# Performance work log

Measured on AMD Instinct MI355X. Metric: run time of the kernel, lower is better.

Reference implementation:

```python
import jax, jax.numpy as jnp
import numpy as np

HEADS = 16
WINDOW = 256
OVERLAP = WINDOW // 8  # 32, matches window_size // 8


def setup_inputs() -> dict:
    key = jax.random.key(0)
    ks = jax.random.split(key, 8)
    n, L, E = 4, 4096, 1024
    d = E // HEADS
    return {
        "values": jax.random.normal(ks[0], (n, L, E), jnp.float32),
        "keys": jax.random.normal(ks[1], (n, L, E), jnp.float32),
        "queries": jax.random.normal(ks[2], (n, L, E), jnp.float32),
        "mask": jnp.ones((n, L), jnp.int32),
        "Wv": jax.random.normal(ks[3], (d, d), jnp.float32) * 0.125,
        "Wk": jax.random.normal(ks[4], (d, d), jnp.float32) * 0.125,
        "Wq": jax.random.normal(ks[5], (d, d), jnp.float32) * 0.125,
        "Wf": jax.random.normal(ks[6], (E, E), jnp.float32) * 0.03125,
        "bf": jnp.zeros((E,), jnp.float32),
    }


def reference(values, keys, queries, mask, Wv, Wk, Wq, Wf, bf):
    n, L, E = queries.shape
    d = E // HEADS
    nW = L // WINDOW            # number of (non-overlapping) query windows
    K = WINDOW + 2 * OVERLAP    # halo-extended key window length

    # per-head linear projections (torch Linear: x @ W^T)
    v = jnp.einsum('nlhd,ed->nlhe', values.reshape(n, L, HEADS, d), Wv)
    k = jnp.einsum('nlhd,ed->nlhe', keys.reshape(n, L, HEADS, d), Wk)
    q = jnp.einsum('nlhd,ed->nlhe', queries.reshape(n, L, HEADS, d), Wq)

    # pad keys/values by the halo; invalid (padded) positions masked with -inf
    kp = jnp.pad(k, ((0, 0), (OVERLAP, OVERLAP), (0, 0), (0, 0)))
    vp = jnp.pad(v, ((0, 0), (OVERLAP, OVERLAP), (0, 0), (0, 0)))
    idx = jnp.arange(nW)[:, None] * WINDOW + jnp.arange(K)[None, :]  # [nW, K] padded coords
    kw = kp[:, idx]  # [n, nW, K, h, d]
    vw = vp[:, idx]
    qw = q.reshape(n, nW, WINDOW, HEADS, d)

    en = jnp.einsum('nwqhd,nwkhd->nwhqk', qw, kw)  # [n, nW, h, WINDOW, K]
    # query-row mask fill (original: masked_fill with -1e10 before scaling)
    qmask = mask.reshape(n, nW, WINDOW)
    en = jnp.where(qmask[:, :, None, :, None] == 0, jnp.float32(-1e10), en)
    # halo positions outside the true sequence get exactly zero weight (= slicing)
    key_valid = (idx >= OVERLAP) & (idx < OVERLAP + L)  # [nW, K]
    en = jnp.where(key_valid[None, :, None, None, :], en, -jnp.inf)

    att = jax.nn.softmax(en / (d ** 0.5), axis=-1)
    out = jnp.einsum('nwhqk,nwkhd->nwqhd', att, vw).reshape(n, L, E)
    return out @ Wf.T + bf
```

## Files before the change

### kernel.cpp

```cpp
#include <hip/hip_runtime.h>
#include <hip/hip_bf16.h>
#include <stdint.h>

typedef unsigned int uint;
typedef unsigned short ushort;

#define NB 4
#define SL 4096
#define EMB 1024
#define NH 16
#define DH 64
#define WIN 256
#define OVL 32
#define NW 16
#define NTOK (NB * SL)

typedef __attribute__((ext_vector_type(8))) short short8;
typedef __attribute__((ext_vector_type(4))) float float4v;

#define AS1 __attribute__((address_space(1)))
#define AS3 __attribute__((address_space(3)))

__device__ __forceinline__ float bf2f(ushort s) { return __uint_as_float((uint)s << 16); }
__device__ __forceinline__ ushort f2bf(float x) {
  uint u = __float_as_uint(x);
  u += 0x7fffu + ((u >> 16) & 1u);
  return (ushort)(u >> 16);
}
__device__ __forceinline__ uint packbf(float a, float b) {
  return (uint)f2bf(a) | ((uint)f2bf(b) << 16);
}

__global__ __launch_bounds__(256) void qkv_proj_mfma(
    const float* __restrict__ qin, const float* __restrict__ kin,
    const float* __restrict__ vin,
    const float* __restrict__ Wq, const float* __restrict__ Wk,
    const float* __restrict__ Wv,
    ushort* __restrict__ qo, ushort* __restrict__ ko, ushort* __restrict__ vo) {
  __shared__ alignas(16) ushort sx[256 * 72];
  __shared__ alignas(16) ushort sw[64 * 72];
  const int t = threadIdx.x;
  const int wid = t >> 6, lane = t & 63, quad = lane >> 4, l16 = lane & 15;
  const int p = blockIdx.z, h = blockIdx.y;
  const int tok0 = blockIdx.x * 256;

  const float* src = (p == 0) ? qin : ((p == 1) ? kin : vin);
  const float* W   = (p == 0) ? Wq  : ((p == 1) ? Wk  : Wv);
  ushort* dst      = (p == 0) ? qo  : ((p == 1) ? ko  : vo);

  for (int i = t; i < 1024; i += 256) {
    int e = i >> 4, c4 = i & 15;
    float4 f = *(const float4*)(W + e * 64 + c4 * 4);
    uint2 u;
    u.x = packbf(f.x, f.y);
    u.y = packbf(f.z, f.w);
    *(uint2*)&sw[e * 72 + c4 * 4] = u;
  }
  for (int i = t; i < 4096; i += 256) {
    int tok = i >> 4, c4 = i & 15;
    float4 f = *(const float4*)(src + (size_t)(tok0 + tok) * EMB + h * DH + c4 * 4);
    uint2 u;
    u.x = packbf(f.x, f.y);
    u.y = packbf(f.z, f.w);
    *(uint2*)&sx[tok * 72 + c4 * 4] = u;
  }
  __syncthreads();

  short8 wa[4][2], xb[4][2];
#pragma unroll
  for (int mt = 0; mt < 4; ++mt)
#pragma unroll
    for (int kh = 0; kh < 2; ++kh)
      wa[mt][kh] = *(const short8*)&sw[(mt * 16 + l16) * 72 + kh * 32 + quad * 8];
#pragma unroll
  for (int nt = 0; nt < 4; ++nt)
#pragma unroll
    for (int kh = 0; kh < 2; ++kh)
      xb[nt][kh] = *(const short8*)&sx[(wid * 64 + nt * 16 + l16) * 72 + kh * 32 + quad * 8];

  float4v acc[4][4];
#pragma unroll
  for (int i = 0; i < 4; ++i)
#pragma unroll
    for (int j = 0; j < 4; ++j) acc[i][j] = (float4v){0.f, 0.f, 0.f, 0.f};
#pragma unroll
  for (int kh = 0; kh < 2; ++kh)
#pragma unroll
    for (int mt = 0; mt < 4; ++mt)
#pragma unroll
      for (int nt = 0; nt < 4; ++nt)
        acc[mt][nt] = __builtin_amdgcn_mfma_f32_16x16x32_bf16(
            wa[mt][kh], xb[nt][kh], acc[mt][nt], 0, 0, 0);

  __syncthreads();
#pragma unroll
  for (int mt = 0; mt < 4; ++mt)
#pragma unroll
    for (int nt = 0; nt < 4; ++nt) {
      uint2 u;
      u.x = packbf(acc[mt][nt][0], acc[mt][nt][1]);
      u.y = packbf(acc[mt][nt][2], acc[mt][nt][3]);
      *(uint2*)&sx[(wid * 64 + nt * 16 + l16) * 72 + mt * 16 + quad * 4] = u;
    }
  __syncthreads();

  {
    const int tokg = tok0 + t;
    const int nb = tokg >> 12, l = tokg & 4095;
    uint4* orow = (uint4*)(dst + ((size_t)(nb * NH + h) * SL + l) * DH);
#pragma unroll
    for (int j = 0; j < 8; ++j) orow[j] = *(const uint4*)&sx[t * 72 + j * 8];
  }
}

__global__ __launch_bounds__(256, 3) void attn_win_mfma(
    const ushort* __restrict__ qws, const ushort* __restrict__ kws,
    const ushort* __restrict__ vws, const int* __restrict__ mask,
    ushort* __restrict__ att) {
  __shared__ alignas(16) ushort sk[64 * 72];
  __shared__ alignas(16) ushort svT[64 * 72];
  __shared__ alignas(16) ushort sp[4][64 * 40];

  const int t = threadIdx.x;
  const int wid = t >> 6, lane = t & 63, quad = lane >> 4, l16 = lane & 15;
  const int bid = blockIdx.x;
  const int h = bid & 15, w = (bid >> 4) & 15, nb = bid >> 8;
  const size_t headbase = (size_t)(nb * NH + h) * SL;
  const int q0 = w * WIN + wid * 64;

  const float CSC = 0.18033688f;
  float sc[4];
#pragma unroll
  for (int qt = 0; qt < 4; ++qt)
    sc[qt] = mask[nb * SL + q0 + qt * 16 + l16] ? CSC : 0.f;

  short8 qf[4][2];
#pragma unroll
  for (int qt = 0; qt < 4; ++qt)
#pragma unroll
    for (int kd = 0; kd < 2; ++kd)
      qf[qt][kd] = *(const short8*)(qws + (headbase + q0 + qt * 16 + l16) * DH +
                                    kd * 32 + quad * 8);

  float4v Of[4][4];
#pragma unroll
  for (int dt = 0; dt < 4; ++dt)
#pragma unroll
    for (int qt = 0; qt < 4; ++qt) Of[dt][qt] = (float4v){0.f, 0.f, 0.f, 0.f};
  float lsum[4] = {0.f, 0.f, 0.f, 0.f};

  ushort* spw = &sp[wid][0];
  const int gk0 = w * WIN - OVL;

  for (int c = 0; c < 5; ++c) {
    __syncthreads();
    const int cbase = gk0 + c * 64;
    for (int s = t; s < 512; s += 256) {
      int key = s & 63, dj = s >> 6;
      int gk = cbase + key;
      uint4 kq = make_uint4(0u, 0u, 0u, 0u);
      uint4 vq = make_uint4(0u, 0u, 0u, 0u);
      if ((unsigned)gk < (unsigned)SL) {
        kq = *(const uint4*)(kws + (headbase + gk) * DH + dj * 8);
        vq = *(const uint4*)(vws + (headbase + gk) * DH + dj * 8);
      }
      *(uint4*)&sk[key * 72 + dj * 8] = kq;
      svT[(dj * 8 + 0) * 72 + key] = (ushort)(vq.x & 0xffffu);
      svT[(dj * 8 + 1) * 72 + key] = (ushort)(vq.x >> 16);
      svT[(dj * 8 + 2) * 72 + key] = (ushort)(vq.y & 0xffffu);
      svT[(dj * 8 + 3) * 72 + key] = (ushort)(vq.y >> 16);
      svT[(dj * 8 + 4) * 72 + key] = (ushort)(vq.z & 0xffffu);
      svT[(dj * 8 + 5) * 72 + key] = (ushort)(vq.z >> 16);
      svT[(dj * 8 + 6) * 72 + key] = (ushort)(vq.w & 0xffffu);
      svT[(dj * 8 + 7) * 72 + key] = (ushort)(vq.w >> 16);
    }
    __syncthreads();

    const bool kmask = (cbase < 0) || (cbase + 64 > SL);

#pragma unroll
    for (int khk = 0; khk < 2; ++khk) {
      float4v Sf[2][4];
#pragma unroll
      for (int kt = 0; kt < 2; ++kt)
#pragma unroll
        for (int qt = 0; qt < 4; ++qt) Sf[kt][qt] = (float4v){0.f, 0.f, 0.f, 0.f};
#pragma unroll
      for (int kd = 0; kd < 2; ++kd) {
        short8 kf[2];
#pragma unroll
        for (int kt = 0; kt < 2; ++kt)
          kf[kt] = *(const short8*)&sk[(khk * 32 + kt * 16 + l16) * 72 +
                                       kd * 32 + quad * 8];
#pragma unroll
        for (int kt = 0; kt < 2; ++kt)
#pragma unroll
          for (int qt = 0; qt < 4; ++qt)
            Sf[kt][qt] = __builtin_amdgcn_mfma_f32_16x16x32_bf16(
                kf[kt], qf[qt][kd], Sf[kt][qt], 0, 0, 0);
      }

#pragma unroll
      for (int kt = 0; kt < 2; ++kt)
#pragma unroll
        for (int qt = 0; qt < 4; ++qt) {
          float p[4];
#pragma unroll
          for (int r = 0; r < 4; ++r)
            p[r] = exp2f(Sf[kt][qt][r] * sc[qt]);
          if (kmask) {
#pragma unroll
            for (int r = 0; r < 4; ++r) {
              const int gkey = cbase + khk * 32 + kt * 16 + quad * 4 + r;
              if ((unsigned)gkey >= (unsigned)SL) p[r] = 0.f;
            }
          }
          uint2 u;
          u.x = packbf(p[0], p[1]);
          u.y = packbf(p[2], p[3]);
          lsum[qt] += (bf2f((ushort)(u.x & 0xffffu)) + bf2f((ushort)(u.x >> 16))) +
                      (bf2f((ushort)(u.y & 0xffffu)) + bf2f((ushort)(u.y >> 16)));
          *(uint2*)&spw[(qt * 16 + l16) * 40 + kt * 16 + quad * 4] = u;
        }

      short8 vf[4], pf[4];
#pragma unroll
      for (int dt = 0; dt < 4; ++dt)
        vf[dt] = *(const short8*)&svT[(dt * 16 + l16) * 72 + khk * 32 + quad * 8];
#pragma unroll
      for (int qt = 0; qt < 4; ++qt)
        pf[qt] = *(const short8*)&spw[(qt * 16 + l16) * 40 + quad * 8];
#pragma unroll
      for (int dt = 0; dt < 4; ++dt)
#pragma unroll
        for (int qt = 0; qt < 4; ++qt)
          Of[dt][qt] = __builtin_amdgcn_mfma_f32_16x16x32_bf16(
              vf[dt], pf[qt], Of[dt][qt], 0, 0, 0);
    }
  }

#pragma unroll
  for (int qt = 0; qt < 4; ++qt) {
    lsum[qt] += __shfl_xor(lsum[qt], 16);
    lsum[qt] += __shfl_xor(lsum[qt], 32);
  }

#pragma unroll
  for (int qt = 0; qt < 4; ++qt) {
    const float inv = 1.f / lsum[qt];
    const size_t token = (size_t)nb * SL + q0 + qt * 16 + l16;
#pragma unroll
    for (int dt = 0; dt < 4; ++dt) {
      uint2 u;
      u.x = packbf(Of[dt][qt][0] * inv, Of[dt][qt][1] * inv);
      u.y = packbf(Of[dt][qt][2] * inv, Of[dt][qt][3] * inv);
      *(uint2*)(att + token * EMB + h * DH + dt * 16 + quad * 4) = u;
    }
  }
}

__global__ __launch_bounds__(256) void wf_cvt(const float* __restrict__ Wf,
                                              ushort* __restrict__ o) {
  const int i = blockIdx.x * 256 + threadIdx.x;
  float4 f = ((const float4*)Wf)[i];
  uint2 u;
  u.x = packbf(f.x, f.y);
  u.y = packbf(f.z, f.w);
  ((uint2*)o)[i] = u;
}

#define GBK 64
__global__ __launch_bounds__(256) void final_gemm_mfma(
    const ushort* __restrict__ A, const ushort* __restrict__ Bt,
    const float* __restrict__ bias, float* __restrict__ C) {
  __shared__ alignas(16) ushort sA[128 * GBK];
  __shared__ alignas(16) ushort sB[128 * GBK];
  const int t = threadIdx.x;
  const int wid = t >> 6, lane = t & 63, quad = lane >> 4, l16 = lane & 15;
  const int n0 = blockIdx.x * 128, m0 = blockIdx.y * 128;
  const int wm = (wid & 1) * 64, wn = (wid >> 1) * 64;

  float4v acc[4][4];
#pragma unroll
  for (int i = 0; i < 4; ++i)
#pragma unroll
    for (int j = 0; j < 4; ++j) acc[i][j] = (float4v){0.f, 0.f, 0.f, 0.f};

  const int arow = lane >> 3;
  const int acol = (lane & 7) * 8;

  for (int k0 = 0; k0 < EMB; k0 += GBK) {
    __syncthreads();
#pragma unroll
    for (int seg = 0; seg < 4; ++seg) {
      const int r = wid * 32 + seg * 8;
      __builtin_amdgcn_global_load_lds(
          (AS1 const void*)(A + (size_t)(m0 + r + arow) * EMB + k0 + acol),
          (AS3 void*)&sA[r * GBK], 16, 0, 0);
      __builtin_amdgcn_global_load_lds(
          (AS1 const void*)(Bt + (size_t)(n0 + r + arow) * EMB + k0 + acol),
          (AS3 void*)&sB[r * GBK], 16, 0, 0);
    }
    __syncthreads();
#pragma unroll
    for (int kk = 0; kk < GBK; kk += 32) {
      short8 af[4], bfr[4];
#pragma unroll
      for (int i = 0; i < 4; ++i)
        af[i] = *(const short8*)&sA[(wm + i * 16 + l16) * GBK + kk + quad * 8];
#pragma unroll
      for (int j = 0; j < 4; ++j)
        bfr[j] = *(const short8*)&sB[(wn + j * 16 + l16) * GBK + kk + quad * 8];
#pragma unroll
      for (int i = 0; i < 4; ++i)
#pragma unroll
        for (int j = 0; j < 4; ++j)
          acc[i][j] = __builtin_amdgcn_mfma_f32_16x16x32_bf16(af[i], bfr[j],
                                                              acc[i][j], 0, 0, 0);
    }
  }

  float bv[4];
#pragma unroll
  for (int j = 0; j < 4; ++j) bv[j] = bias[n0 + wn + j * 16 + l16];
#pragma unroll
  for (int i = 0; i < 4; ++i)
#pragma unroll
    for (int j = 0; j < 4; ++j)
#pragma unroll
      for (int r = 0; r < 4; ++r)
        C[(size_t)(m0 + wm + i * 16 + quad * 4 + r) * EMB + n0 + wn + j * 16 +
          l16] = acc[i][j][r] + bv[j];
}

extern "C" void kernel_launch(void* const* d_in, const int* in_sizes, int n_in,
                              void* d_out, int out_size, void* d_ws,
                              size_t ws_size, hipStream_t stream) {
  const float* values  = (const float*)d_in[0];
  const float* keys    = (const float*)d_in[1];
  const float* queries = (const float*)d_in[2];
  const int*   mask    = (const int*)d_in[3];
  const float* Wv = (const float*)d_in[4];
  const float* Wk = (const float*)d_in[5];
  const float* Wq = (const float*)d_in[6];
  const float* Wf = (const float*)d_in[7];
  const float* bfv = (const float*)d_in[8];
  float* out = (float*)d_out;

  ushort* ws = (ushort*)d_ws;
  ushort* q_ws = ws;
  ushort* k_ws = ws + (size_t)16777216;
  ushort* v_ws = ws + (size_t)33554432;
  ushort* a_ws = ws + (size_t)50331648;
  ushort* wf_bf = q_ws;

  qkv_proj_mfma<<<dim3(NTOK / 256, NH, 3), 256, 0, stream>>>(
      queries, keys, values, Wq, Wk, Wv, q_ws, k_ws, v_ws);
  attn_win_mfma<<<NB * NW * NH, 256, 0, stream>>>(q_ws, k_ws, v_ws, mask, a_ws);
  wf_cvt<<<1024, 256, 0, stream>>>(Wf, wf_bf);
  final_gemm_mfma<<<dim3(EMB / 128, NTOK / 128), 256, 0, stream>>>(a_ws, wf_bf,
                                                                   bfv, out);
}
```

Baseline: 465.9 us.

## Store V pre-transposed from projection and stage attention output through LDS

The projection kernel now writes V in a head-major transposed [d, L] layout by computing the transposed product and staging it through LDS. This lets the attention kernel load V^T tiles with vector loads instead of scalar scattered LDS writes. The attention output is also staged in shared memory so each thread writes a full 128-byte row, and the projection grid order is swapped so heads vary fastest. The cost is extra syncs and LDS traffic in the epilogues, and V halo loads now work at 8-key granularity.

```diff
diff --git a/kernel.cpp b/kernel.cpp
--- a/kernel.cpp
+++ b/kernel.cpp
@@ -37,12 +37,16 @@
     const float* __restrict__ Wq, const float* __restrict__ Wk,
     const float* __restrict__ Wv,
     ushort* __restrict__ qo, ushort* __restrict__ ko, ushort* __restrict__ vo) {
-  __shared__ alignas(16) ushort sx[256 * 72];
-  __shared__ alignas(16) ushort sw[64 * 72];
+  __shared__ alignas(16) ushort smem[256 * 72 + 64 * 72];
+  ushort* sx = smem;
+  ushort* sw = smem + 256 * 72;
+  ushort* sxT = smem;
+
   const int t = threadIdx.x;
   const int wid = t >> 6, lane = t & 63, quad = lane >> 4, l16 = lane & 15;
-  const int p = blockIdx.z, h = blockIdx.y;
-  const int tok0 = blockIdx.x * 256;
+  const int p = blockIdx.z, h = blockIdx.x;
+  const int tok0 = blockIdx.y * 256;
+  const int nb = tok0 >> 12, l0 = tok0 & 4095;
 
   const float* src = (p == 0) ? qin : ((p == 1) ? kin : vin);
   const float* W   = (p == 0) ? Wq  : ((p == 1) ? Wk  : Wv);
@@ -66,50 +70,72 @@
   }
   __syncthreads();
 
-  short8 wa[4][2], xb[4][2];
-#pragma unroll
-  for (int mt = 0; mt < 4; ++mt)
+  short8 wfr[4][2], xfr[4][2];
+#pragma unroll
+  for (int et = 0; et < 4; ++et)
 #pragma unroll
     for (int kh = 0; kh < 2; ++kh)
-      wa[mt][kh] = *(const short8*)&sw[(mt * 16 + l16) * 72 + kh * 32 + quad * 8];
-#pragma unroll
-  for (int nt = 0; nt < 4; ++nt)
+      wfr[et][kh] = *(const short8*)&sw[(et * 16 + l16) * 72 + kh * 32 + quad * 8];
+#pragma unroll
+  for (int tt = 0; tt < 4; ++tt)
 #pragma unroll
     for (int kh = 0; kh < 2; ++kh)
-      xb[nt][kh] = *(const short8*)&sx[(wid * 64 + nt * 16 + l16) * 72 + kh * 32 + quad * 8];
+      xfr[tt][kh] = *(const short8*)&sx[(wid * 64 + tt * 16 + l16) * 72 + kh * 32 + quad * 8];
 
   float4v acc[4][4];
 #pragma unroll
   for (int i = 0; i < 4; ++i)
 #pragma unroll
     for (int j = 0; j < 4; ++j) acc[i][j] = (float4v){0.f, 0.f, 0.f, 0.f};
-#pragma unroll
-  for (int kh = 0; kh < 2; ++kh)
-#pragma unroll
-    for (int mt = 0; mt < 4; ++mt)
-#pragma unroll
-      for (int nt = 0; nt < 4; ++nt)
-        acc[mt][nt] = __builtin_amdgcn_mfma_f32_16x16x32_bf16(
-            wa[mt][kh], xb[nt][kh], acc[mt][nt], 0, 0, 0);
-
-  __syncthreads();
-#pragma unroll
-  for (int mt = 0; mt < 4; ++mt)
-#pragma unroll
-    for (int nt = 0; nt < 4; ++nt) {
-      uint2 u;
-      u.x = packbf(acc[mt][nt][0], acc[mt][nt][1]);
-      u.y = packbf(acc[mt][nt][2], acc[mt][nt][3]);
-      *(uint2*)&sx[(wid * 64 + nt * 16 + l16) * 72 + mt * 16 + quad * 4] = u;
-    }
-  __syncthreads();
-
-  {
-    const int tokg = tok0 + t;
-    const int nb = tokg >> 12, l = tokg & 4095;
-    uint4* orow = (uint4*)(dst + ((size_t)(nb * NH + h) * SL + l) * DH);
+
+  if (p != 2) {
+#pragma unroll
+    for (int kh = 0; kh < 2; ++kh)
+#pragma unroll
+      for (int et = 0; et < 4; ++et)
+#pragma unroll
+        for (int tt = 0; tt < 4; ++tt)
+          acc[et][tt] = __builtin_amdgcn_mfma_f32_16x16x32_bf16(
+              wfr[et][kh], xfr[tt][kh], acc[et][tt], 0, 0, 0);
+    __syncthreads();
+#pragma unroll
+    for (int et = 0; et < 4; ++et)
+#pragma unroll
+      for (int tt = 0; tt < 4; ++tt) {
+        uint2 u;
+        u.x = packbf(acc[et][tt][0], acc[et][tt][1]);
+        u.y = packbf(acc[et][tt][2], acc[et][tt][3]);
+        *(uint2*)&sx[(wid * 64 + tt * 16 + l16) * 72 + et * 16 + quad * 4] = u;
+      }
+    __syncthreads();
+    uint4* orow = (uint4*)(dst + ((size_t)(nb * NH + h) * SL + l0 + t) * DH);
 #pragma unroll
     for (int j = 0; j < 8; ++j) orow[j] = *(const uint4*)&sx[t * 72 + j * 8];
+  } else {
+#pragma unroll
+    for (int kh = 0; kh < 2; ++kh)
+#pragma unroll
+      for (int tt = 0; tt < 4; ++tt)
+#pragma unroll
+        for (int et = 0; et < 4; ++et)
+          acc[tt][et] = __builtin_amdgcn_mfma_f32_16x16x32_bf16(
+              xfr[tt][kh], wfr[et][kh], acc[tt][et], 0, 0, 0);
+    __syncthreads();
+#pragma unroll
+    for (int tt = 0; tt < 4; ++tt)
+#pragma unroll
+      for (int et = 0; et < 4; ++et) {
+        uint2 u;
+        u.x = packbf(acc[tt][et][0], acc[tt][et][1]);
+        u.y = packbf(acc[tt][et][2], acc[tt][et][3]);
+        *(uint2*)&sxT[(et * 16 + l16) * 264 + wid * 64 + tt * 16 + quad * 4] = u;
+      }
+    __syncthreads();
+    const int e = t >> 2, part = t & 3;
+    uint4* orow = (uint4*)(dst + ((size_t)(nb * NH + h) * DH + e) * SL + l0 + part * 64);
+    const ushort* srow = &sxT[e * 264 + part * 64];
+#pragma unroll
+    for (int j = 0; j < 8; ++j) orow[j] = *(const uint4*)&srow[j * 8];
   }
 }
 
@@ -117,15 +143,18 @@
     const ushort* __restrict__ qws, const ushort* __restrict__ kws,
     const ushort* __restrict__ vws, const int* __restrict__ mask,
     ushort* __restrict__ att) {
-  __shared__ alignas(16) ushort sk[64 * 72];
-  __shared__ alignas(16) ushort svT[64 * 72];
-  __shared__ alignas(16) ushort sp[4][64 * 40];
+  __shared__ alignas(16) ushort smem[19456];
+  ushort* sk  = smem;
+  ushort* svT = smem + 4608;
+  ushort* sp  = smem + 9216;
+  ushort* sO  = smem;
 
   const int t = threadIdx.x;
   const int wid = t >> 6, lane = t & 63, quad = lane >> 4, l16 = lane & 15;
   const int bid = blockIdx.x;
   const int h = bid & 15, w = (bid >> 4) & 15, nb = bid >> 8;
   const size_t headbase = (size_t)(nb * NH + h) * SL;
+  const ushort* vT = vws + (size_t)(nb * NH + h) * DH * SL;
   const int q0 = w * WIN + wid * 64;
 
   const float CSC = 0.18033688f;
@@ -149,30 +178,28 @@
     for (int qt = 0; qt < 4; ++qt) Of[dt][qt] = (float4v){0.f, 0.f, 0.f, 0.f};
   float lsum[4] = {0.f, 0.f, 0.f, 0.f};
 
-  ushort* spw = &sp[wid][0];
+  ushort* spw = &sp[wid * 2560];
   const int gk0 = w * WIN - OVL;
 
   for (int c = 0; c < 5; ++c) {
     __syncthreads();
     const int cbase = gk0 + c * 64;
     for (int s = t; s < 512; s += 256) {
-      int key = s & 63, dj = s >> 6;
-      int gk = cbase + key;
-      uint4 kq = make_uint4(0u, 0u, 0u, 0u);
-      uint4 vq = make_uint4(0u, 0u, 0u, 0u);
-      if ((unsigned)gk < (unsigned)SL) {
-        kq = *(const uint4*)(kws + (headbase + gk) * DH + dj * 8);
-        vq = *(const uint4*)(vws + (headbase + gk) * DH + dj * 8);
-      }
-      *(uint4*)&sk[key * 72 + dj * 8] = kq;
-      svT[(dj * 8 + 0) * 72 + key] = (ushort)(vq.x & 0xffffu);
-      svT[(dj * 8 + 1) * 72 + key] = (ushort)(vq.x >> 16);
-      svT[(dj * 8 + 2) * 72 + key] = (ushort)(vq.y & 0xffffu);
-      svT[(dj * 8 + 3) * 72 + key] = (ushort)(vq.y >> 16);
-      svT[(dj * 8 + 4) * 72 + key] = (ushort)(vq.z & 0xffffu);
-      svT[(dj * 8 + 5) * 72 + key] = (ushort)(vq.z >> 16);
-      svT[(dj * 8 + 6) * 72 + key] = (ushort)(vq.w & 0xffffu);
-      svT[(dj * 8 + 7) * 72 + key] = (ushort)(vq.w >> 16);
+      const int r = s >> 3, c8 = (s & 7) * 8;
+      {
+        const int gk = cbase + r;
+        uint4 kq = make_uint4(0u, 0u, 0u, 0u);
+        if ((unsigned)gk < (unsigned)SL)
+          kq = *(const uint4*)(kws + (headbase + gk) * DH + c8);
+        *(uint4*)&sk[r * 72 + c8] = kq;
+      }
+      {
+        const int gkc = cbase + c8;
+        uint4 vq = make_uint4(0u, 0u, 0u, 0u);
+        if (gkc >= 0 && gkc + 8 <= SL)
+          vq = *(const uint4*)(vT + (size_t)r * SL + gkc);
+        *(uint4*)&svT[r * 72 + c8] = vq;
+      }
     }
     __syncthreads();
 
@@ -206,8 +233,7 @@
         for (int qt = 0; qt < 4; ++qt) {
           float p[4];
 #pragma unroll
-          for (int r = 0; r < 4; ++r)
-            p[r] = exp2f(Sf[kt][qt][r] * sc[qt]);
+          for (int r = 0; r < 4; ++r) p[r] = exp2f(Sf[kt][qt][r] * sc[qt]);
           if (kmask) {
 #pragma unroll
             for (int r = 0; r < 4; ++r) {
@@ -245,17 +271,24 @@
     lsum[qt] += __shfl_xor(lsum[qt], 32);
   }
 
+  __syncthreads();
 #pragma unroll
   for (int qt = 0; qt < 4; ++qt) {
     const float inv = 1.f / lsum[qt];
-    const size_t token = (size_t)nb * SL + q0 + qt * 16 + l16;
 #pragma unroll
     for (int dt = 0; dt < 4; ++dt) {
       uint2 u;
       u.x = packbf(Of[dt][qt][0] * inv, Of[dt][qt][1] * inv);
       u.y = packbf(Of[dt][qt][2] * inv, Of[dt][qt][3] * inv);
-      *(uint2*)(att + token * EMB + h * DH + dt * 16 + quad * 4) = u;
-    }
+      *(uint2*)&sO[(wid * 64 + qt * 16 + l16) * 72 + dt * 16 + quad * 4] = u;
+    }
+  }
+  __syncthreads();
+  {
+    const size_t token = (size_t)nb * SL + w * WIN + t;
+    uint4* orow = (uint4*)(att + token * EMB + h * DH);
+#pragma unroll
+    for (int j = 0; j < 8; ++j) orow[j] = *(const uint4*)&sO[t * 72 + j * 8];
   }
 }
 
@@ -354,7 +387,7 @@
   ushort* a_ws = ws + (size_t)50331648;
   ushort* wf_bf = q_ws;
 
-  qkv_proj_mfma<<<dim3(NTOK / 256, NH, 3), 256, 0, stream>>>(
+  qkv_proj_mfma<<<dim3(NH, NTOK / 256, 3), 256, 0, stream>>>(
       queries, keys, values, Wq, Wk, Wv, q_ws, k_ws, v_ws);
   attn_win_mfma<<<NB * NW * NH, 256, 0, stream>>>(q_ws, k_ws, v_ws, mask, a_ws);
   wf_cvt<<<1024, 256, 0, stream>>>(Wf, wf_bf);
```

New measurement: 426.6 us. 8.4% less time.
